# Kernel optimization log

Hardware: AMD Instinct MI355X
Metric: run time of the kernel (lower is better)

Reference implementation:

```python
import jax, jax.numpy as jnp
import numpy as np

D_MODEL = 1024
TEMPERATURE = 1.0

def setup_inputs() -> dict:
    key = jax.random.key(0)
    ks = jax.random.split(key, 9)
    B, NQ, NK, D = 4, 2048, 2048, D_MODEL
    s = 1.0 / np.sqrt(D)
    return {
        "Q": jax.random.normal(ks[0], (B, NQ, D), jnp.float32),
        "K": jax.random.normal(ks[1], (B, NK, D), jnp.float32),
        "V": jax.random.normal(ks[2], (B, NK, D), jnp.float32),
        "Wq": jax.random.normal(ks[3], (D, D), jnp.float32) * s,
        "bq": jax.random.normal(ks[4], (D,), jnp.float32) * 0.01,
        "Wk": jax.random.normal(ks[5], (D, D), jnp.float32) * s,
        "bk": jax.random.normal(ks[6], (D,), jnp.float32) * 0.01,
        "Wv": jax.random.normal(ks[7], (D, D), jnp.float32) * s,
        "bv": jax.random.normal(ks[8], (D,), jnp.float32) * 0.01,
    }

def reference(Q, K, V, Wq, bq, Wk, bk, Wv, bv):
    # torch nn.Linear: y = x @ W.T + b
    Qp = Q @ Wq.T + bq  # [B, NQ, D]
    Kp = K @ Wk.T + bk  # [B, NK, D]
    Vp = V @ Wv.T + bv  # [B, NK, D]

    # use_kl=True branch, vectorized:
    # kl[b,i,j] = D_KL(softmax(Kp[b,j]) || softmax(Qp[b,i]))
    #           = sum_d pK*(log pK - log pQ) = -H(pK_j) - pK_j . log pQ_i
    logpQ = jax.nn.log_softmax(Qp, axis=-1)  # [B, NQ, D]
    logpK = jax.nn.log_softmax(Kp, axis=-1)  # [B, NK, D]
    pK = jnp.exp(logpK)
    neg_ent_K = jnp.sum(pK * logpK, axis=-1)            # [B, NK], = -H(pK)
    cross = jnp.einsum('bjd,bid->bij', pK, logpQ)       # [B, NQ, NK]
    kl = neg_ent_K[:, None, :] - cross                  # [B, NQ, NK]
    scores = -kl / TEMPERATURE

    attn = jax.nn.softmax(scores, axis=-1)              # [B, NQ, NK]
    out = jnp.einsum('bij,bjd->bid', attn, Vp)          # [B, NQ, D]
    return out, attn
```

## Files before the change

kernel.cpp:

```cpp
#include <hip/hip_runtime.h>
#include <math.h>

#define D_MODEL 1024
#define NQS 2048
#define NKS 2048
#define BATCH 4

typedef __attribute__((ext_vector_type(8))) short bf16x8;
typedef __attribute__((ext_vector_type(4))) float f32x4;

#define AS1 __attribute__((address_space(1)))
#define AS3 __attribute__((address_space(3)))

__device__ __forceinline__ unsigned short f2bf(float f) {
  unsigned u = __builtin_bit_cast(unsigned, f);
  u = (u + 0x7FFF + ((u >> 16) & 1)) >> 16;
  return (unsigned short)u;
}
__device__ __forceinline__ float bf2f(unsigned short s) {
  return __builtin_bit_cast(float, ((unsigned)s) << 16);
}

__global__ __launch_bounds__(256) void cvt3_k(
    const float* __restrict__ s0, const float* __restrict__ s1,
    const float* __restrict__ s2, short* __restrict__ d0,
    short* __restrict__ d1, short* __restrict__ d2, int n8)
{
  const int z = blockIdx.z;
  const float* src = z == 0 ? s0 : (z == 1 ? s1 : s2);
  short* dst = z == 0 ? d0 : (z == 1 ? d1 : d2);
  int i = blockIdx.x * 256 + threadIdx.x;
  if (i >= n8) return;
  const float4 a = *(const float4*)&src[(long)i * 8];
  const float4 b = *(const float4*)&src[(long)i * 8 + 4];
  bf16x8 o;
  o[0] = (short)f2bf(a.x); o[1] = (short)f2bf(a.y);
  o[2] = (short)f2bf(a.z); o[3] = (short)f2bf(a.w);
  o[4] = (short)f2bf(b.x); o[5] = (short)f2bf(b.y);
  o[6] = (short)f2bf(b.z); o[7] = (short)f2bf(b.w);
  *(bf16x8*)&dst[(long)i * 8] = o;
}

__device__ __forceinline__ void gemm_tile_body(
    const short* __restrict__ Ab, const short* __restrict__ Bb,
    const float* __restrict__ bias, float bscale, float* __restrict__ Cf,
    short* __restrict__ Cbf, int N, int K)
{
  __shared__ short As[128 * 32];
  __shared__ short Bs[128 * 32];
  const int gm = blockIdx.y * 128, gn = blockIdx.x * 128;
  const int t = threadIdx.x;
  const int lane = t & 63, w = t >> 6;
  const int wm = w >> 1, wn = w & 1;

  const int srow = lane >> 2, sq = lane & 3;
  const short* ga0 = Ab + (long)(gm + w * 32 + srow) * K + sq * 8;
  const short* ga1 = Ab + (long)(gm + w * 32 + 16 + srow) * K + sq * 8;
  const short* gb0 = Bb + (long)(gn + w * 32 + srow) * K + sq * 8;
  const short* gb1 = Bb + (long)(gn + w * 32 + 16 + srow) * K + sq * 8;
  short* la0 = As + (w * 2 + 0) * 512;
  short* la1 = As + (w * 2 + 1) * 512;
  short* lb0 = Bs + (w * 2 + 0) * 512;
  short* lb1 = Bs + (w * 2 + 1) * 512;

  const int frow = lane & 15, fq = lane >> 4;

  f32x4 acc[4][4] = {};

  for (int k0 = 0; k0 < K; k0 += 32) {
    __builtin_amdgcn_global_load_lds((const AS1 void*)(ga0 + k0),
                                     (AS3 void*)la0, 16, 0, 0);
    __builtin_amdgcn_global_load_lds((const AS1 void*)(ga1 + k0),
                                     (AS3 void*)la1, 16, 0, 0);
    __builtin_amdgcn_global_load_lds((const AS1 void*)(gb0 + k0),
                                     (AS3 void*)lb0, 16, 0, 0);
    __builtin_amdgcn_global_load_lds((const AS1 void*)(gb1 + k0),
                                     (AS3 void*)lb1, 16, 0, 0);
    __syncthreads();
    bf16x8 af[4], bfm[4];
#pragma unroll
    for (int mi = 0; mi < 4; ++mi)
      af[mi] = *(const bf16x8*)&As[(wm * 64 + mi * 16 + frow) * 32 + fq * 8];
#pragma unroll
    for (int ni = 0; ni < 4; ++ni)
      bfm[ni] = *(const bf16x8*)&Bs[(wn * 64 + ni * 16 + frow) * 32 + fq * 8];
#pragma unroll
    for (int mi = 0; mi < 4; ++mi)
#pragma unroll
      for (int ni = 0; ni < 4; ++ni)
        acc[mi][ni] = __builtin_amdgcn_mfma_f32_16x16x32_bf16(
            af[mi], bfm[ni], acc[mi][ni], 0, 0, 0);
    __syncthreads();
  }

  float bb[4];
#pragma unroll
  for (int ni = 0; ni < 4; ++ni)
    bb[ni] = bias ? bias[gn + wn * 64 + ni * 16 + frow] * bscale : 0.f;

#pragma unroll
  for (int mi = 0; mi < 4; ++mi) {
#pragma unroll
    for (int r = 0; r < 4; ++r) {
      const long row = gm + wm * 64 + mi * 16 + fq * 4 + r;
#pragma unroll
      for (int ni = 0; ni < 4; ++ni) {
        const long col = gn + wn * 64 + ni * 16 + frow;
        float v = acc[mi][ni][r] + bb[ni];
        if (Cf) Cf[row * (long)N + col] = v;
        else    Cbf[row * (long)N + col] = (short)f2bf(v);
      }
    }
  }
}

__global__ __launch_bounds__(256, 4) void mfma_abt_k(
    const short* __restrict__ A, const short* __restrict__ B,
    const float* __restrict__ bias, float bscale, float* __restrict__ Cf,
    short* __restrict__ Cbf, int N, int K, long sA, long sB, long sC,
    long sBias)
{
  const int bz = blockIdx.z;
  gemm_tile_body(A + (long)bz * sA, B + (long)bz * sB,
                 bias ? bias + (long)bz * sBias : nullptr, bscale,
                 Cf ? Cf + (long)bz * sC : nullptr,
                 Cbf ? Cbf + (long)bz * sC : nullptr, N, K);
}

__global__ __launch_bounds__(256, 4) void mfma_proj_k(
    const short* __restrict__ Xq, const short* __restrict__ Xk,
    const short* __restrict__ Xv, const short* __restrict__ Wq,
    const short* __restrict__ Wk, const short* __restrict__ Wv,
    const float* __restrict__ bq, const float* __restrict__ bk,
    const float* __restrict__ bv, short* __restrict__ Oq,
    short* __restrict__ Ok, short* __restrict__ Ov)
{
  const int z = blockIdx.z;
  const short* X = z == 0 ? Xq : (z == 1 ? Xk : Xv);
  const short* W = z == 0 ? Wq : (z == 1 ? Wk : Wv);
  const float* bias = z == 0 ? bq : (z == 1 ? bk : bv);
  short* O = z == 0 ? Oq : (z == 1 ? Ok : Ov);
  gemm_tile_body(X, W, bias, 1.0f, nullptr, O, D_MODEL, D_MODEL);
}

__global__ __launch_bounds__(256) void kstats_k(short* __restrict__ KP,
                                                float* __restrict__ negent)
{
  __shared__ float red[4];
  const long row = blockIdx.x;
  short* x = KP + row * (long)D_MODEL;
  const int t = threadIdx.x;
  short4 raw = *(const short4*)&x[t * 4];
  float v0 = bf2f((unsigned short)raw.x), v1 = bf2f((unsigned short)raw.y);
  float v2 = bf2f((unsigned short)raw.z), v3 = bf2f((unsigned short)raw.w);
  float m = fmaxf(fmaxf(v0, v1), fmaxf(v2, v3));
  for (int o = 32; o; o >>= 1) m = fmaxf(m, __shfl_xor(m, o));
  if ((t & 63) == 0) red[t >> 6] = m;
  __syncthreads();
  m = fmaxf(fmaxf(red[0], red[1]), fmaxf(red[2], red[3]));
  __syncthreads();
  float e0 = __expf(v0 - m), e1 = __expf(v1 - m), e2 = __expf(v2 - m),
        e3 = __expf(v3 - m);
  float s = e0 + e1 + e2 + e3;
  for (int o = 32; o; o >>= 1) s += __shfl_xor(s, o);
  if ((t & 63) == 0) red[t >> 6] = s;
  __syncthreads();
  s = red[0] + red[1] + red[2] + red[3];
  __syncthreads();
  const float inv = 1.0f / s;
  const float lse = m + __logf(s);
  float p0 = e0 * inv, p1 = e1 * inv, p2 = e2 * inv, p3 = e3 * inv;
  float ne = p0 * (v0 - lse) + p1 * (v1 - lse) + p2 * (v2 - lse) +
             p3 * (v3 - lse);
  for (int o = 32; o; o >>= 1) ne += __shfl_xor(ne, o);
  if ((t & 63) == 0) red[t >> 6] = ne;
  __syncthreads();
  if (t == 0) negent[row] = red[0] + red[1] + red[2] + red[3];
  short4 pw;
  pw.x = (short)f2bf(p0); pw.y = (short)f2bf(p1);
  pw.z = (short)f2bf(p2); pw.w = (short)f2bf(p3);
  *(short4*)&x[t * 4] = pw;
}

__global__ __launch_bounds__(256) void asoftmax_k(float* __restrict__ S,
                                                  short* __restrict__ Sbf)
{
  __shared__ float red[4];
  const long row = blockIdx.x;
  float* x = S + row * (long)NKS;
  short* y = Sbf + row * (long)NKS;
  const int t = threadIdx.x;
  float4 v0 = *(const float4*)&x[t * 4];
  float4 v1 = *(const float4*)&x[1024 + t * 4];
  float m = fmaxf(fmaxf(fmaxf(v0.x, v0.y), fmaxf(v0.z, v0.w)),
                  fmaxf(fmaxf(v1.x, v1.y), fmaxf(v1.z, v1.w)));
  for (int o = 32; o; o >>= 1) m = fmaxf(m, __shfl_xor(m, o));
  if ((t & 63) == 0) red[t >> 6] = m;
  __syncthreads();
  m = fmaxf(fmaxf(red[0], red[1]), fmaxf(red[2], red[3]));
  __syncthreads();
  float4 e0 = {__expf(v0.x - m), __expf(v0.y - m), __expf(v0.z - m),
               __expf(v0.w - m)};
  float4 e1 = {__expf(v1.x - m), __expf(v1.y - m), __expf(v1.z - m),
               __expf(v1.w - m)};
  float s = e0.x + e0.y + e0.z + e0.w + e1.x + e1.y + e1.z + e1.w;
  for (int o = 32; o; o >>= 1) s += __shfl_xor(s, o);
  if ((t & 63) == 0) red[t >> 6] = s;
  __syncthreads();
  s = red[0] + red[1] + red[2] + red[3];
  const float inv = 1.0f / s;
  float4 p0 = {e0.x * inv, e0.y * inv, e0.z * inv, e0.w * inv};
  float4 p1 = {e1.x * inv, e1.y * inv, e1.z * inv, e1.w * inv};
  *(float4*)&x[t * 4] = p0;
  *(float4*)&x[1024 + t * 4] = p1;
  short4 b0, b1;
  b0.x = (short)f2bf(p0.x); b0.y = (short)f2bf(p0.y);
  b0.z = (short)f2bf(p0.z); b0.w = (short)f2bf(p0.w);
  b1.x = (short)f2bf(p1.x); b1.y = (short)f2bf(p1.y);
  b1.z = (short)f2bf(p1.z); b1.w = (short)f2bf(p1.w);
  *(short4*)&y[t * 4] = b0;
  *(short4*)&y[1024 + t * 4] = b1;
}

__global__ __launch_bounds__(256) void transpose_k(const short* __restrict__ src,
                                                   short* __restrict__ dst)
{
  __shared__ short tile[64][68];
  const int j0 = blockIdx.x * 64;
  const int d0 = blockIdx.y * 64;
  const int t = threadIdx.x;
  const int r = t >> 2, c = t & 3;
#pragma unroll
  for (int i = 0; i < 4; ++i)
    *(short4*)&tile[r][c * 16 + i * 4] =
        *(const short4*)&src[(long)(j0 + r) * D_MODEL + d0 + c * 16 + i * 4];
  __syncthreads();
  const long b = j0 >> 11;
  const int jj = j0 & 2047;
#pragma unroll
  for (int i = 0; i < 4; ++i) {
    short4 o;
    o.x = tile[c * 16 + i * 4 + 0][r];
    o.y = tile[c * 16 + i * 4 + 1][r];
    o.z = tile[c * 16 + i * 4 + 2][r];
    o.w = tile[c * 16 + i * 4 + 3][r];
    *(short4*)&dst[b * ((long)D_MODEL * NKS) + (long)(d0 + r) * NKS + jj +
                   c * 16 + i * 4] = o;
  }
}

extern "C" void kernel_launch(void* const* d_in, const int* in_sizes, int n_in,
                              void* d_out, int out_size, void* d_ws,
                              size_t ws_size, hipStream_t stream)
{
  const float* Q = (const float*)d_in[0];
  const float* K = (const float*)d_in[1];
  const float* V = (const float*)d_in[2];
  const float* Wq = (const float*)d_in[3];
  const float* bq = (const float*)d_in[4];
  const float* Wk = (const float*)d_in[5];
  const float* bk = (const float*)d_in[6];
  const float* Wv = (const float*)d_in[7];
  const float* bv = (const float*)d_in[8];

  float* out = (float*)d_out;
  float* attn = out + (long)BATCH * NQS * D_MODEL;

  const long SZ = (long)BATCH * NQS * D_MODEL;
  short* ws = (short*)d_ws;
  short* Qbf = ws;
  short* Kbf = ws + SZ;
  short* Vbf = ws + 2 * SZ;
  short* Qp  = ws + 3 * SZ;
  short* pK  = ws + 4 * SZ;
  short* Vp  = ws + 5 * SZ;
  float* negent = (float*)(ws + 6 * SZ);
  short* attn_bf = ws;
  short* Vpt = ws + 2 * SZ;

  short* Wqb = (short*)attn;
  short* Wkb = Wqb + (long)D_MODEL * D_MODEL;
  short* Wvb = Wkb + (long)D_MODEL * D_MODEL;

  dim3 blk(256);
  const int n8x = (int)(SZ / 8);
  const int n8w = D_MODEL * D_MODEL / 8;

  cvt3_k<<<dim3(n8x / 256, 1, 3), blk, 0, stream>>>(Q, K, V, Qbf, Kbf, Vbf,
                                                    n8x);
  cvt3_k<<<dim3(n8w / 256, 1, 3), blk, 0, stream>>>(Wq, Wk, Wv, Wqb, Wkb, Wvb,
                                                    n8w);

  dim3 gp(D_MODEL / 128, (BATCH * NQS) / 128, 3);
  mfma_proj_k<<<gp, blk, 0, stream>>>(Qbf, Kbf, Vbf, Wqb, Wkb, Wvb, bq, bk,
                                      bv, Qp, pK, Vp);

  kstats_k<<<dim3(BATCH * NKS), blk, 0, stream>>>(pK, negent);

  transpose_k<<<dim3((BATCH * NKS) / 64, D_MODEL / 64), blk, 0, stream>>>(Vp,
                                                                          Vpt);

  dim3 gs(NKS / 128, NQS / 128, BATCH);
  mfma_abt_k<<<gs, blk, 0, stream>>>(
      Qp, pK, negent, -1.0f, attn, nullptr, NKS, D_MODEL,
      (long)NQS * D_MODEL, (long)NKS * D_MODEL, (long)NQS * NKS, NKS);

  asoftmax_k<<<dim3(BATCH * NQS), blk, 0, stream>>>(attn, attn_bf);

  dim3 go(D_MODEL / 128, NQS / 128, BATCH);
  mfma_abt_k<<<go, blk, 0, stream>>>(
      attn_bf, Vpt, nullptr, 0.f, out, nullptr, D_MODEL, NKS,
      (long)NQS * NKS, (long)D_MODEL * NKS, (long)NQS * D_MODEL, 0);
}
```

Baseline: 405.0 us.

## Deepen GEMM K-step to 64 with two LDS stages and reorder block rasterization

The shared GEMM body now loads two 32-wide K slices per iteration into separate LDS buffers before a single barrier, halving the number of barrier pairs and issuing more global loads in flight. It also swaps the grid mapping for the projection and output GEMMs so that consecutive blocks walk along M instead of N, which changes which operand tiles share L2. The cost is doubled LDS per block, which may reduce occupancy below the launch-bound target.

After: 378.8 us. 6.5% less time.

```diff
diff --git a/kernel.cpp b/kernel.cpp
--- a/kernel.cpp
+++ b/kernel.cpp
@@ -44,52 +44,57 @@
 __device__ __forceinline__ void gemm_tile_body(
     const short* __restrict__ Ab, const short* __restrict__ Bb,
     const float* __restrict__ bias, float bscale, float* __restrict__ Cf,
-    short* __restrict__ Cbf, int N, int K)
-{
-  __shared__ short As[128 * 32];
-  __shared__ short Bs[128 * 32];
-  const int gm = blockIdx.y * 128, gn = blockIdx.x * 128;
+    short* __restrict__ Cbf, int N, int K, int gm, int gn)
+{
+  __shared__ short As[2][128 * 32];
+  __shared__ short Bs[2][128 * 32];
   const int t = threadIdx.x;
   const int lane = t & 63, w = t >> 6;
   const int wm = w >> 1, wn = w & 1;
 
   const int srow = lane >> 2, sq = lane & 3;
-  const short* ga0 = Ab + (long)(gm + w * 32 + srow) * K + sq * 8;
-  const short* ga1 = Ab + (long)(gm + w * 32 + 16 + srow) * K + sq * 8;
-  const short* gb0 = Bb + (long)(gn + w * 32 + srow) * K + sq * 8;
-  const short* gb1 = Bb + (long)(gn + w * 32 + 16 + srow) * K + sq * 8;
-  short* la0 = As + (w * 2 + 0) * 512;
-  short* la1 = As + (w * 2 + 1) * 512;
-  short* lb0 = Bs + (w * 2 + 0) * 512;
-  short* lb1 = Bs + (w * 2 + 1) * 512;
+  const short* gA0 = Ab + (long)(gm + w * 32 + srow) * K + sq * 8;
+  const short* gA1 = Ab + (long)(gm + w * 32 + 16 + srow) * K + sq * 8;
+  const short* gB0 = Bb + (long)(gn + w * 32 + srow) * K + sq * 8;
+  const short* gB1 = Bb + (long)(gn + w * 32 + 16 + srow) * K + sq * 8;
+  const int seg0 = (w * 2 + 0) * 512, seg1 = (w * 2 + 1) * 512;
 
   const int frow = lane & 15, fq = lane >> 4;
 
   f32x4 acc[4][4] = {};
 
-  for (int k0 = 0; k0 < K; k0 += 32) {
-    __builtin_amdgcn_global_load_lds((const AS1 void*)(ga0 + k0),
-                                     (AS3 void*)la0, 16, 0, 0);
-    __builtin_amdgcn_global_load_lds((const AS1 void*)(ga1 + k0),
-                                     (AS3 void*)la1, 16, 0, 0);
-    __builtin_amdgcn_global_load_lds((const AS1 void*)(gb0 + k0),
-                                     (AS3 void*)lb0, 16, 0, 0);
-    __builtin_amdgcn_global_load_lds((const AS1 void*)(gb1 + k0),
-                                     (AS3 void*)lb1, 16, 0, 0);
+  for (int k0 = 0; k0 < K; k0 += 64) {
+#pragma unroll
+    for (int p = 0; p < 2; ++p) {
+      const int ko = k0 + p * 32;
+      __builtin_amdgcn_global_load_lds((const AS1 void*)(gA0 + ko),
+                                       (AS3 void*)(&As[p][seg0]), 16, 0, 0);
+      __builtin_amdgcn_global_load_lds((const AS1 void*)(gA1 + ko),
+                                       (AS3 void*)(&As[p][seg1]), 16, 0, 0);
+      __builtin_amdgcn_global_load_lds((const AS1 void*)(gB0 + ko),
+                                       (AS3 void*)(&Bs[p][seg0]), 16, 0, 0);
+      __builtin_amdgcn_global_load_lds((const AS1 void*)(gB1 + ko),
+                                       (AS3 void*)(&Bs[p][seg1]), 16, 0, 0);
+    }
     __syncthreads();
-    bf16x8 af[4], bfm[4];
-#pragma unroll
-    for (int mi = 0; mi < 4; ++mi)
-      af[mi] = *(const bf16x8*)&As[(wm * 64 + mi * 16 + frow) * 32 + fq * 8];
-#pragma unroll
-    for (int ni = 0; ni < 4; ++ni)
-      bfm[ni] = *(const bf16x8*)&Bs[(wn * 64 + ni * 16 + frow) * 32 + fq * 8];
-#pragma unroll
-    for (int mi = 0; mi < 4; ++mi)
+#pragma unroll
+    for (int p = 0; p < 2; ++p) {
+      bf16x8 af[4], bfm[4];
+#pragma unroll
+      for (int mi = 0; mi < 4; ++mi)
+        af[mi] =
+            *(const bf16x8*)&As[p][(wm * 64 + mi * 16 + frow) * 32 + fq * 8];
 #pragma unroll
       for (int ni = 0; ni < 4; ++ni)
-        acc[mi][ni] = __builtin_amdgcn_mfma_f32_16x16x32_bf16(
-            af[mi], bfm[ni], acc[mi][ni], 0, 0, 0);
+        bfm[ni] =
+            *(const bf16x8*)&Bs[p][(wn * 64 + ni * 16 + frow) * 32 + fq * 8];
+#pragma unroll
+      for (int mi = 0; mi < 4; ++mi)
+#pragma unroll
+        for (int ni = 0; ni < 4; ++ni)
+          acc[mi][ni] = __builtin_amdgcn_mfma_f32_16x16x32_bf16(
+              af[mi], bfm[ni], acc[mi][ni], 0, 0, 0);
+    }
     __syncthreads();
   }
 
@@ -118,13 +123,15 @@
     const short* __restrict__ A, const short* __restrict__ B,
     const float* __restrict__ bias, float bscale, float* __restrict__ Cf,
     short* __restrict__ Cbf, int N, int K, long sA, long sB, long sC,
-    long sBias)
+    long sBias, int swap)
 {
   const int bz = blockIdx.z;
+  const int gm = (swap ? blockIdx.x : blockIdx.y) * 128;
+  const int gn = (swap ? blockIdx.y : blockIdx.x) * 128;
   gemm_tile_body(A + (long)bz * sA, B + (long)bz * sB,
                  bias ? bias + (long)bz * sBias : nullptr, bscale,
                  Cf ? Cf + (long)bz * sC : nullptr,
-                 Cbf ? Cbf + (long)bz * sC : nullptr, N, K);
+                 Cbf ? Cbf + (long)bz * sC : nullptr, N, K, gm, gn);
 }
 
 __global__ __launch_bounds__(256, 4) void mfma_proj_k(
@@ -140,7 +147,8 @@
   const short* W = z == 0 ? Wq : (z == 1 ? Wk : Wv);
   const float* bias = z == 0 ? bq : (z == 1 ? bk : bv);
   short* O = z == 0 ? Oq : (z == 1 ? Ok : Ov);
-  gemm_tile_body(X, W, bias, 1.0f, nullptr, O, D_MODEL, D_MODEL);
+  gemm_tile_body(X, W, bias, 1.0f, nullptr, O, D_MODEL, D_MODEL,
+                 blockIdx.x * 128, blockIdx.y * 128);
 }
 
 __global__ __launch_bounds__(256) void kstats_k(short* __restrict__ KP,
@@ -291,7 +299,7 @@
   cvt3_k<<<dim3(n8w / 256, 1, 3), blk, 0, stream>>>(Wq, Wk, Wv, Wqb, Wkb, Wvb,
                                                     n8w);
 
-  dim3 gp(D_MODEL / 128, (BATCH * NQS) / 128, 3);
+  dim3 gp((BATCH * NQS) / 128, D_MODEL / 128, 3);
   mfma_proj_k<<<gp, blk, 0, stream>>>(Qbf, Kbf, Vbf, Wqb, Wkb, Wvb, bq, bk,
                                       bv, Qp, pK, Vp);
 
@@ -303,12 +311,12 @@
   dim3 gs(NKS / 128, NQS / 128, BATCH);
   mfma_abt_k<<<gs, blk, 0, stream>>>(
       Qp, pK, negent, -1.0f, attn, nullptr, NKS, D_MODEL,
-      (long)NQS * D_MODEL, (long)NKS * D_MODEL, (long)NQS * NKS, NKS);
+      (long)NQS * D_MODEL, (long)NKS * D_MODEL, (long)NQS * NKS, NKS, 0);
 
   asoftmax_k<<<dim3(BATCH * NQS), blk, 0, stream>>>(attn, attn_bf);
 
-  dim3 go(D_MODEL / 128, NQS / 128, BATCH);
+  dim3 go(NQS / 128, D_MODEL / 128, BATCH);
   mfma_abt_k<<<go, blk, 0, stream>>>(
       attn_bf, Vpt, nullptr, 0.f, out, nullptr, D_MODEL, NKS,
-      (long)NQS * NKS, (long)D_MODEL * NKS, (long)NQS * D_MODEL, 0);
-}
+      (long)NQS * NKS, (long)D_MODEL * NKS, (long)NQS * D_MODEL, 0, 1);
+}
```
